# Kernel tuning notes

Measured on AMD Instinct MI355X. Metric: run time of the kernel, lower is better.

Reference implementation:

```python
import jax, jax.numpy as jnp
import numpy as np

B, D, U, BR, IU, HID = 1024, 2048, 4096, 4, 3072, 32


def setup_inputs() -> dict:
    key = jax.random.key(0)
    ks = jax.random.split(key, 12)
    inputs = jax.random.normal(ks[0], (B, D), dtype=jnp.float32)
    # dendritic kernel / bias / delay (glorot-ish scale)
    w = jax.random.normal(ks[1], (D, U, BR), dtype=jnp.float32) * 0.02
    b = jax.random.normal(ks[2], (U, BR), dtype=jnp.float32) * 0.01
    delay = jax.random.normal(ks[3], (D, U, BR), dtype=jnp.float32) * 0.5
    # branch gating dense (softmax applied in reference)
    Wg = jax.random.normal(ks[4], (D, BR), dtype=jnp.float32) * 0.02
    bg = jnp.zeros((BR,), dtype=jnp.float32)
    # DynamicConnectivity attention net: Dense(32, relu) -> Dense(U, sigmoid)
    W1 = jax.random.normal(ks[5], (U, HID), dtype=jnp.float32) * 0.02
    b1 = jnp.zeros((HID,), dtype=jnp.float32)
    W2 = jax.random.normal(ks[6], (HID, U), dtype=jnp.float32) * 0.02
    b2 = jnp.zeros((U,), dtype=jnp.float32)
    # non-trainable state
    neuron_mask = jnp.concatenate([jnp.ones((IU,), jnp.float32), jnp.zeros((U - IU,), jnp.float32)])
    neuron_activation_avg = jax.random.uniform(ks[7], (U,), dtype=jnp.float32) * 0.1
    return {"inputs": inputs, "w": w, "b": b, "delay": delay, "Wg": Wg, "bg": bg,
            "W1": W1, "b1": b1, "W2": W2, "b2": b2,
            "neuron_mask": neuron_mask, "neuron_activation_avg": neuron_activation_avg}


def reference(inputs, w, b, delay, Wg, bg, W1, b1, W2, b2, neuron_mask, neuron_activation_avg):
    # sigmoid-gated weights, 3-way tensordot -> [B, U, BR]
    w_mod = w * jax.nn.sigmoid(delay)
    branch_outputs = jnp.einsum('bd,duk->buk', inputs, w_mod) + b
    # per-branch softmax gating from the input, soft combine over branches
    gating = jax.nn.softmax(inputs @ Wg + bg, axis=-1)            # [B, BR]
    z_combined = jnp.einsum('buk,bk->bu', branch_outputs, gating)  # [B, U]
    # dynamic connectivity from neuron activation EMA state: [1, U]
    h = jax.nn.relu(neuron_activation_avg[None, :] @ W1 + b1)
    connectivity = jax.nn.sigmoid(h @ W2 + b2)                     # [1, U]
    z_modulated = z_combined * connectivity * neuron_mask[None, :]
    a = jax.nn.relu(z_modulated)
    return a
```

## Files before the change

kernel.cpp:

```cpp
#include <hip/hip_runtime.h>
#include <cstdint>
#include <cstddef>

typedef __bf16 bf16;
typedef __bf16 bf16x4 __attribute__((ext_vector_type(4)));
typedef __bf16 bf16x8 __attribute__((ext_vector_type(8)));
typedef float f32x4 __attribute__((ext_vector_type(4)));

#define B_SZ 1024
#define D_SZ 2048
#define U_SZ 4096
#define BR_SZ 4
#define N_SZ (U_SZ * BR_SZ)

#define WS_WT 0
#define WS_A (64u * 1024u * 1024u)
#define WS_GAT (WS_A + 4u * 1024u * 1024u)
#define WS_H (WS_GAT + 16384u)

__device__ __forceinline__ float sigmoidf_(float x) { return 1.f / (1.f + __expf(-x)); }

__device__ __forceinline__ uint32_t pack2_(float lo, float hi) {
  union { bf16 h[2]; uint32_t u; } cv;
  cv.h[0] = (bf16)lo; cv.h[1] = (bf16)hi;
  return cv.u;
}

__global__ void k01_prep(const float* __restrict__ in, bf16* __restrict__ wa,
                         const float* __restrict__ Wg, const float* __restrict__ bg,
                         float* __restrict__ gat, float* __restrict__ wsh) {
  int row = blockIdx.x, tid = threadIdx.x;
  if (row == 0 && tid < 32) wsh[tid] = 0.f;
  const float* ir = in + (size_t)row * D_SZ;
  float a0 = 0, a1 = 0, a2 = 0, a3 = 0;
#pragma unroll
  for (int c = 0; c < 2; c++) {
    int d = c * 1024 + tid * 4;
    float4 x = *(const float4*)(ir + d);
    bf16x4 o;
    o[0] = (bf16)x.x; o[1] = (bf16)x.y; o[2] = (bf16)x.z; o[3] = (bf16)x.w;
    *(bf16x4*)(wa + (size_t)row * D_SZ + d) = o;
    const float xs[4] = {x.x, x.y, x.z, x.w};
#pragma unroll
    for (int j = 0; j < 4; j++) {
      float4 wg = ((const float4*)Wg)[d + j];
      a0 += xs[j] * wg.x; a1 += xs[j] * wg.y; a2 += xs[j] * wg.z; a3 += xs[j] * wg.w;
    }
  }
#pragma unroll
  for (int off = 32; off; off >>= 1) {
    a0 += __shfl_down(a0, off); a1 += __shfl_down(a1, off);
    a2 += __shfl_down(a2, off); a3 += __shfl_down(a3, off);
  }
  __shared__ float red[4][4];
  int wv = tid >> 6, ln = tid & 63;
  if (ln == 0) { red[wv][0] = a0; red[wv][1] = a1; red[wv][2] = a2; red[wv][3] = a3; }
  __syncthreads();
  if (tid == 0) {
    float s0 = red[0][0] + red[1][0] + red[2][0] + red[3][0] + bg[0];
    float s1 = red[0][1] + red[1][1] + red[2][1] + red[3][1] + bg[1];
    float s2 = red[0][2] + red[1][2] + red[2][2] + red[3][2] + bg[2];
    float s3 = red[0][3] + red[1][3] + red[2][3] + red[3][3] + bg[3];
    float m = fmaxf(fmaxf(s0, s1), fmaxf(s2, s3));
    float e0 = __expf(s0 - m), e1 = __expf(s1 - m), e2 = __expf(s2 - m), e3 = __expf(s3 - m);
    float inv = 1.f / (e0 + e1 + e2 + e3);
    ((float4*)gat)[row] = make_float4(e0 * inv, e1 * inv, e2 * inv, e3 * inv);
  }
}

__global__ void k2a_h(const float* __restrict__ avg, const float* __restrict__ W1,
                      float* __restrict__ wsh) {
  int t = threadIdx.x;
  int h = t & 31, seg = t >> 5;
  int u0 = blockIdx.x * 64 + seg * 8;
  float p = 0.f;
#pragma unroll
  for (int j = 0; j < 8; j++) {
    int u = u0 + j;
    p += avg[u] * W1[u * 32 + h];
  }
  __shared__ float red[8][32];
  red[seg][h] = p;
  __syncthreads();
  if (t < 32) {
    float s = 0.f;
#pragma unroll
    for (int sg = 0; sg < 8; sg++) s += red[sg][t];
    atomicAdd(&wsh[t], s);
  }
}

#define K3P 33
__global__ __launch_bounds__(256) void k3_wmod_t(const float* __restrict__ w,
                                                 const float* __restrict__ delay,
                                                 bf16* __restrict__ wt) {
  __shared__ uint32_t buf[2][64 * K3P];
  int tid = threadIdx.x;
  int n0 = blockIdx.x * 64;
  int d0 = blockIdx.y * 256;
  int d2 = tid >> 4, n4 = tid & 15;
  int p2n = tid >> 3, p2o = tid & 7;

  float4 rw[4], rd[4];

#define K3_LOAD(t)                                                         \
  {                                                                        \
    _Pragma("unroll") for (int pass = 0; pass < 2; pass++) {               \
      int d = d0 + (t) * 64 + pass * 32 + d2 * 2;                          \
      size_t g = (size_t)d * N_SZ + n0 + n4 * 4;                           \
      rw[pass * 2 + 0] = *(const float4*)(w + g);                          \
      rw[pass * 2 + 1] = *(const float4*)(w + g + N_SZ);                   \
      rd[pass * 2 + 0] = *(const float4*)(delay + g);                      \
      rd[pass * 2 + 1] = *(const float4*)(delay + g + N_SZ);               \
    }                                                                      \
  }
#define K3_WRITE(bsel)                                                     \
  {                                                                        \
    _Pragma("unroll") for (int pass = 0; pass < 2; pass++) {               \
      const float* fw0 = (const float*)&rw[pass * 2 + 0];                  \
      const float* fw1 = (const float*)&rw[pass * 2 + 1];                  \
      const float* fd0 = (const float*)&rd[pass * 2 + 0];                  \
      const float* fd1 = (const float*)&rd[pass * 2 + 1];                  \
      _Pragma("unroll") for (int j = 0; j < 4; j++) {                      \
        float lo = fw0[j] * sigmoidf_(fd0[j]);                             \
        float hi = fw1[j] * sigmoidf_(fd1[j]);                             \
        buf[bsel][(n4 * 4 + j) * K3P + pass * 16 + d2] = pack2_(lo, hi);   \
      }                                                                    \
    }                                                                      \
  }
#define K3_STORE(t, bsel)                                                  \
  {                                                                        \
    int dt = d0 + (t) * 64;                                                \
    _Pragma("unroll") for (int pass = 0; pass < 2; pass++) {               \
      int n = pass * 32 + p2n;                                             \
      const uint32_t* r = &buf[bsel][n * K3P + p2o * 4];                   \
      uint4 v;                                                             \
      v.x = r[0]; v.y = r[1]; v.z = r[2]; v.w = r[3];                      \
      *(uint4*)(wt + (size_t)(n0 + n) * D_SZ + dt + p2o * 8) = v;          \
    }                                                                      \
  }

  K3_LOAD(0);
  K3_WRITE(0);
#pragma unroll
  for (int t = 0; t < 4; t++) {
    __syncthreads();
    if (t < 3) K3_LOAD(t + 1);
    K3_STORE(t, (t & 1));
    if (t < 3) K3_WRITE(((t + 1) & 1));
  }
}

__global__ __launch_bounds__(256, 2) void k4_gemm(
    const bf16* __restrict__ A, const bf16* __restrict__ Bt,
    const float* __restrict__ gating, const float* __restrict__ bias,
    const float* __restrict__ wsh, const float* __restrict__ b1,
    const float* __restrict__ W2, const float* __restrict__ b2,
    const float* __restrict__ mask, float* __restrict__ out) {
  __shared__ bf16 Al[128 * 64];
  __shared__ bf16 Bl[128 * 64];
  __shared__ float gat[128 * 4];
  __shared__ float conn_l[32];
  int tid = threadIdx.x;
  int lane = tid & 63, wave = tid >> 6;
  int bid = blockIdx.x;
  int xcd = bid & 7, p = bid >> 3;
  int mt = p & 7, nt = (xcd << 4) | (p >> 3);
  int m0 = mt * 128, n0 = nt * 128;
  int wm = (wave & 1) * 64, wn = (wave >> 1) * 64;
  int quad = lane >> 4, row16 = lane & 15;
  int r7 = row16 & 7;

  f32x4 acc[4][4];
  const f32x4 z4 = {0.f, 0.f, 0.f, 0.f};
#pragma unroll
  for (int i = 0; i < 4; i++)
#pragma unroll
    for (int j = 0; j < 4; j++) acc[i][j] = z4;

  if (tid < 128) *(float4*)&gat[tid * 4] = *(const float4*)&gating[(m0 + tid) * 4];
  if (tid < 32) {
    int u = (n0 >> 2) + tid;
    float s = b2[u];
#pragma unroll
    for (int h = 0; h < 32; h++) s += fmaxf(wsh[h] + b1[h], 0.f) * W2[h * U_SZ + u];
    conn_l[tid] = sigmoidf_(s) * mask[u];
  }

  int srow = lane >> 3;
  int scol = ((lane & 7) ^ srow) * 8;
  for (int kt = 0; kt < 32; kt++) {
    int k0 = kt * 64;
#pragma unroll
    for (int c = 0; c < 4; c++) {
      int rb = wave * 32 + c * 8;
      const bf16* ga = A + (size_t)(m0 + rb + srow) * D_SZ + k0 + scol;
      __builtin_amdgcn_global_load_lds(
          (const __attribute__((address_space(1))) void*)ga,
          (__attribute__((address_space(3))) void*)(Al + rb * 64), 16, 0, 0);
      const bf16* gb = Bt + (size_t)(n0 + rb + srow) * D_SZ + k0 + scol;
      __builtin_amdgcn_global_load_lds(
          (const __attribute__((address_space(1))) void*)gb,
          (__attribute__((address_space(3))) void*)(Bl + rb * 64), 16, 0, 0);
    }
    __syncthreads();
#pragma unroll
    for (int kk = 0; kk < 64; kk += 32) {
      int csw = (((kk >> 3) + quad) ^ r7) * 8;
      bf16x8 af[4], bfr[4];
#pragma unroll
      for (int i = 0; i < 4; i++)
        af[i] = *(const bf16x8*)&Al[(wm + i * 16 + row16) * 64 + csw];
#pragma unroll
      for (int j = 0; j < 4; j++)
        bfr[j] = *(const bf16x8*)&Bl[(wn + j * 16 + row16) * 64 + csw];
#pragma unroll
      for (int i = 0; i < 4; i++)
#pragma unroll
        for (int j = 0; j < 4; j++)
          acc[i][j] = __builtin_amdgcn_mfma_f32_16x16x32_bf16(af[i], bfr[j], acc[i][j], 0, 0, 0);
    }
    __syncthreads();
  }

  int k = lane & 3;
#pragma unroll
  for (int j = 0; j < 4; j++) {
    int n_l = wn + j * 16 + row16;
    int n_g = n0 + n_l;
    int u = n_g >> 2;
    float bv = bias[n_g];
    float cv = conn_l[n_l >> 2];
#pragma unroll
    for (int i = 0; i < 4; i++) {
#pragma unroll
      for (int r = 0; r < 4; r++) {
        int r_l = wm + i * 16 + quad * 4 + r;
        float g = gat[r_l * 4 + k];
        float v = (acc[i][j][r] + bv) * g;
        v += __shfl_xor(v, 1);
        v += __shfl_xor(v, 2);
        if (k == 0) out[(size_t)(m0 + r_l) * U_SZ + u] = fmaxf(v * cv, 0.f);
      }
    }
  }
}

extern "C" void kernel_launch(void* const* d_in, const int* in_sizes, int n_in,
                              void* d_out, int out_size, void* d_ws, size_t ws_size,
                              hipStream_t stream) {
  const float* inputs = (const float*)d_in[0];
  const float* w = (const float*)d_in[1];
  const float* bb = (const float*)d_in[2];
  const float* delay = (const float*)d_in[3];
  const float* Wg = (const float*)d_in[4];
  const float* bg = (const float*)d_in[5];
  const float* W1 = (const float*)d_in[6];
  const float* b1 = (const float*)d_in[7];
  const float* W2 = (const float*)d_in[8];
  const float* b2 = (const float*)d_in[9];
  const float* mask = (const float*)d_in[10];
  const float* avg = (const float*)d_in[11];
  float* out = (float*)d_out;
  char* ws = (char*)d_ws;
  bf16* wt = (bf16*)(ws + WS_WT);
  bf16* wa = (bf16*)(ws + WS_A);
  float* gat = (float*)(ws + WS_GAT);
  float* wsh = (float*)(ws + WS_H);

  hipLaunchKernelGGL(k01_prep, dim3(B_SZ), dim3(256), 0, stream, inputs, wa, Wg, bg, gat, wsh);
  hipLaunchKernelGGL(k2a_h, dim3(U_SZ / 64), dim3(256), 0, stream, avg, W1, wsh);
  hipLaunchKernelGGL(k3_wmod_t, dim3(N_SZ / 64, D_SZ / 256), dim3(256), 0, stream, w, delay, wt);
  hipLaunchKernelGGL(k4_gemm, dim3((B_SZ / 128) * (N_SZ / 128)), dim3(256), 0, stream, wa, wt, gat, bb, wsh, b1, W2, b2, mask, out);
}
```

Before: 389.6 us.

## Store GEMM operands in K-blocked 64-wide panels and simplify weight transpose kernel

Both GEMM operands (bf16 inputs and transposed modulated weights) are now stored in a K-panel layout where each 64-element K slice of all rows is contiguous. Each 128x64 tile load in the GEMM then reads one contiguous 16 KB region instead of 128 strided row segments. The weight-modulation transpose kernel is rewritten to handle 128 D rows per block in one pass without double buffering, with a wider padded LDS buffer. This trades the software pipelining inside the prep kernel for more blocks and simpler stores.

```diff
diff --git a/kernel.cpp b/kernel.cpp
--- a/kernel.cpp
+++ b/kernel.cpp
@@ -39,7 +39,7 @@
     float4 x = *(const float4*)(ir + d);
     bf16x4 o;
     o[0] = (bf16)x.x; o[1] = (bf16)x.y; o[2] = (bf16)x.z; o[3] = (bf16)x.w;
-    *(bf16x4*)(wa + (size_t)row * D_SZ + d) = o;
+    *(bf16x4*)(wa + ((size_t)(d >> 6) * B_SZ + row) * 64 + (d & 63)) = o;
     const float xs[4] = {x.x, x.y, x.z, x.w};
 #pragma unroll
     for (int j = 0; j < 4; j++) {
@@ -90,64 +90,46 @@
   }
 }
 
-#define K3P 33
+#define K3P 66
 __global__ __launch_bounds__(256) void k3_wmod_t(const float* __restrict__ w,
                                                  const float* __restrict__ delay,
                                                  bf16* __restrict__ wt) {
-  __shared__ uint32_t buf[2][64 * K3P];
+  __shared__ uint32_t buf[64 * K3P];
   int tid = threadIdx.x;
   int n0 = blockIdx.x * 64;
-  int d0 = blockIdx.y * 256;
-  int d2 = tid >> 4, n4 = tid & 15;
-  int p2n = tid >> 3, p2o = tid & 7;
-
-  float4 rw[4], rd[4];
-
-#define K3_LOAD(t)                                                         \
-  {                                                                        \
-    _Pragma("unroll") for (int pass = 0; pass < 2; pass++) {               \
-      int d = d0 + (t) * 64 + pass * 32 + d2 * 2;                          \
-      size_t g = (size_t)d * N_SZ + n0 + n4 * 4;                           \
-      rw[pass * 2 + 0] = *(const float4*)(w + g);                          \
-      rw[pass * 2 + 1] = *(const float4*)(w + g + N_SZ);                   \
-      rd[pass * 2 + 0] = *(const float4*)(delay + g);                      \
-      rd[pass * 2 + 1] = *(const float4*)(delay + g + N_SZ);               \
-    }                                                                      \
-  }
-#define K3_WRITE(bsel)                                                     \
-  {                                                                        \
-    _Pragma("unroll") for (int pass = 0; pass < 2; pass++) {               \
-      const float* fw0 = (const float*)&rw[pass * 2 + 0];                  \
-      const float* fw1 = (const float*)&rw[pass * 2 + 1];                  \
-      const float* fd0 = (const float*)&rd[pass * 2 + 0];                  \
-      const float* fd1 = (const float*)&rd[pass * 2 + 1];                  \
-      _Pragma("unroll") for (int j = 0; j < 4; j++) {                      \
-        float lo = fw0[j] * sigmoidf_(fd0[j]);                             \
-        float hi = fw1[j] * sigmoidf_(fd1[j]);                             \
-        buf[bsel][(n4 * 4 + j) * K3P + pass * 16 + d2] = pack2_(lo, hi);   \
-      }                                                                    \
-    }                                                                      \
-  }
-#define K3_STORE(t, bsel)                                                  \
-  {                                                                        \
-    int dt = d0 + (t) * 64;                                                \
-    _Pragma("unroll") for (int pass = 0; pass < 2; pass++) {               \
-      int n = pass * 32 + p2n;                                             \
-      const uint32_t* r = &buf[bsel][n * K3P + p2o * 4];                   \
-      uint4 v;                                                             \
-      v.x = r[0]; v.y = r[1]; v.z = r[2]; v.w = r[3];                      \
-      *(uint4*)(wt + (size_t)(n0 + n) * D_SZ + dt + p2o * 8) = v;          \
-    }                                                                      \
-  }
-
-  K3_LOAD(0);
-  K3_WRITE(0);
-#pragma unroll
-  for (int t = 0; t < 4; t++) {
-    __syncthreads();
-    if (t < 3) K3_LOAD(t + 1);
-    K3_STORE(t, (t & 1));
-    if (t < 3) K3_WRITE(((t + 1) & 1));
+  int d0 = blockIdx.y * 128;
+  int n4 = tid & 15, dh = tid >> 4;
+
+  float4 wv[8], dv[8];
+  const float* wp = w + (size_t)(d0 + dh * 8) * N_SZ + n0 + n4 * 4;
+  const float* dp = delay + (size_t)(d0 + dh * 8) * N_SZ + n0 + n4 * 4;
+#pragma unroll
+  for (int k = 0; k < 8; k++) {
+    wv[k] = *(const float4*)(wp + (size_t)k * N_SZ);
+    dv[k] = *(const float4*)(dp + (size_t)k * N_SZ);
+  }
+#pragma unroll
+  for (int k2 = 0; k2 < 4; k2++) {
+    const float* f0 = (const float*)&wv[2 * k2];
+    const float* f1 = (const float*)&wv[2 * k2 + 1];
+    const float* g0 = (const float*)&dv[2 * k2];
+    const float* g1 = (const float*)&dv[2 * k2 + 1];
+#pragma unroll
+    for (int j = 0; j < 4; j++) {
+      float lo = f0[j] * sigmoidf_(g0[j]);
+      float hi = f1[j] * sigmoidf_(g1[j]);
+      buf[(n4 * 4 + j) * K3P + dh * 4 + k2] = pack2_(lo, hi);
+    }
+  }
+  __syncthreads();
+  int n = tid >> 2, seg = tid & 3;
+  const uint32_t* r = &buf[n * K3P + seg * 16];
+  bf16* dst = wt + ((size_t)((d0 >> 6) + (seg >> 1)) * N_SZ + n0 + n) * 64 + (seg & 1) * 32;
+#pragma unroll
+  for (int q = 0; q < 4; q++) {
+    uint4 v;
+    v.x = r[q * 4 + 0]; v.y = r[q * 4 + 1]; v.z = r[q * 4 + 2]; v.w = r[q * 4 + 3];
+    *(uint4*)(dst + q * 8) = v;
   }
 }
 
@@ -190,15 +172,14 @@
   int srow = lane >> 3;
   int scol = ((lane & 7) ^ srow) * 8;
   for (int kt = 0; kt < 32; kt++) {
-    int k0 = kt * 64;
 #pragma unroll
     for (int c = 0; c < 4; c++) {
       int rb = wave * 32 + c * 8;
-      const bf16* ga = A + (size_t)(m0 + rb + srow) * D_SZ + k0 + scol;
+      const bf16* ga = A + ((size_t)kt * B_SZ + m0 + rb + srow) * 64 + scol;
       __builtin_amdgcn_global_load_lds(
           (const __attribute__((address_space(1))) void*)ga,
           (__attribute__((address_space(3))) void*)(Al + rb * 64), 16, 0, 0);
-      const bf16* gb = Bt + (size_t)(n0 + rb + srow) * D_SZ + k0 + scol;
+      const bf16* gb = Bt + ((size_t)kt * N_SZ + n0 + rb + srow) * 64 + scol;
       __builtin_amdgcn_global_load_lds(
           (const __attribute__((address_space(1))) void*)gb,
           (__attribute__((address_space(3))) void*)(Bl + rb * 64), 16, 0, 0);
@@ -270,6 +251,6 @@
 
   hipLaunchKernelGGL(k01_prep, dim3(B_SZ), dim3(256), 0, stream, inputs, wa, Wg, bg, gat, wsh);
   hipLaunchKernelGGL(k2a_h, dim3(U_SZ / 64), dim3(256), 0, stream, avg, W1, wsh);
-  hipLaunchKernelGGL(k3_wmod_t, dim3(N_SZ / 64, D_SZ / 256), dim3(256), 0, stream, w, delay, wt);
+  hipLaunchKernelGGL(k3_wmod_t, dim3(N_SZ / 64, D_SZ / 128), dim3(256), 0, stream, w, delay, wt);
   hipLaunchKernelGGL(k4_gemm, dim3((B_SZ / 128) * (N_SZ / 128)), dim3(256), 0, stream, wa, wt, gat, bb, wsh, b1, W2, b2, mask, out);
 }
```

Measured after the change: 396.1 us. About the same (+1.7%).
